# Performance work log

Hardware: AMD Instinct MI355X
Metric: run time of the kernel (lower is better)

The kernel has to match this reference:

```python
import jax, jax.numpy as jnp
import numpy as np

HIDDEN = 768
N_HEADS = 12
HEAD_DIM = HIDDEN // N_HEADS  # 64
SEQ = 2048
BATCH = 2
ROPE_BASE = 10000.0


def _rope_cos_sin(seq_len, head_dim):
    inv_freq = 1.0 / (ROPE_BASE ** (jnp.arange(0, head_dim, 2, dtype=jnp.float32) / head_dim))
    t = jnp.arange(seq_len, dtype=jnp.float32)
    freqs = jnp.einsum('s,d->sd', t, inv_freq)          # [S, D/2]
    emb = jnp.concatenate([freqs, freqs], axis=-1)      # [S, D]
    return jnp.cos(emb), jnp.sin(emb)


def _rotate_half(x):
    x1, x2 = jnp.split(x, 2, axis=-1)
    return jnp.concatenate([-x2, x1], axis=-1)


def setup_inputs() -> dict:
    key = jax.random.key(0)
    ks = jax.random.split(key, 6)
    scale = 1.0 / np.sqrt(HIDDEN)
    hidden_states = jax.random.normal(ks[0], (BATCH, SEQ, HIDDEN), dtype=jnp.float32)
    wq = jax.random.normal(ks[1], (HIDDEN, HIDDEN), dtype=jnp.float32) * scale
    wk = jax.random.normal(ks[2], (HIDDEN, HIDDEN), dtype=jnp.float32) * scale
    wv = jax.random.normal(ks[3], (HIDDEN, HIDDEN), dtype=jnp.float32) * scale
    wo = jax.random.normal(ks[4], (HIDDEN, HIDDEN), dtype=jnp.float32) * scale
    # additive causal mask: 0 on/below diagonal, large negative above
    causal = jnp.triu(jnp.full((SEQ, SEQ), -1e9, dtype=jnp.float32), k=1)
    attn_mask = causal[None, None, :, :]
    return {"hidden_states": hidden_states, "wq": wq, "wk": wk, "wv": wv,
            "wo": wo, "attn_mask": attn_mask}


def reference(hidden_states, wq, wk, wv, wo, attn_mask):
    B, S, _ = hidden_states.shape
    # projections (nn.Linear: x @ W.T)
    def proj(w):
        y = jnp.einsum('bsh,oh->bso', hidden_states, w)
        return y.reshape(B, S, N_HEADS, HEAD_DIM).transpose(0, 2, 1, 3)  # [B,H,S,D]
    q, k, v = proj(wq), proj(wk), proj(wv)
    cos, sin = _rope_cos_sin(S, HEAD_DIM)  # [S, D]
    cos = cos[None, None, :, :].astype(hidden_states.dtype)
    sin = sin[None, None, :, :].astype(hidden_states.dtype)
    q = q * cos + _rotate_half(q) * sin
    k = k * cos + _rotate_half(k) * sin
    scores = jnp.einsum('bhqd,bhkd->bhqk', q, k) / np.sqrt(HEAD_DIM)
    scores = scores + attn_mask
    probs = jax.nn.softmax(scores.astype(jnp.float32), axis=-1).astype(q.dtype)
    out = jnp.einsum('bhqk,bhkd->bhqd', probs, v)
    out = out.transpose(0, 2, 1, 3).reshape(B, S, HIDDEN)
    return jnp.einsum('bsh,oh->bso', out, wo)
```

## Files before the change

### kernel.cpp

```cpp
#include <hip/hip_runtime.h>

typedef unsigned short u16;
typedef short short8 __attribute__((ext_vector_type(8)));
typedef float f32x4 __attribute__((ext_vector_type(4)));

static_assert(sizeof(short8) == 16, "short8 must be 16B");

__device__ __forceinline__ u16 f2bf(float f) {
  unsigned u = __float_as_uint(f);
  u += 0x7FFFu + ((u >> 16) & 1u);
  return (u16)(u >> 16);
}
__device__ __forceinline__ float bf2f(u16 h) { return __uint_as_float(((unsigned)h) << 16); }

__device__ __forceinline__ f32x4 mfma_bf16(short8 a, short8 b, f32x4 c) {
  return __builtin_amdgcn_mfma_f32_16x16x32_bf16(a, b, c, 0, 0, 0);
}

__device__ __forceinline__ void gload_lds16(const void* g, void* l) {
  __builtin_amdgcn_global_load_lds((__attribute__((address_space(1))) void*)g,
                                   (__attribute__((address_space(3))) void*)l, 16, 0, 0);
}

__device__ __forceinline__ float exp2v(float x) {
  float r; asm("v_exp_f32 %0, %1" : "=v"(r) : "v"(x)); return r;
}
__device__ __forceinline__ unsigned cvtpk(float lo, float hi) {
  unsigned r; asm("v_cvt_pk_bf16_f32 %0, %1, %2" : "=v"(r) : "v"(lo), "v"(hi)); return r;
}
__device__ __forceinline__ f32x4 vmax4(f32x4 a, f32x4 b) {
  f32x4 r;
  r[0] = fmaxf(a[0], b[0]); r[1] = fmaxf(a[1], b[1]);
  r[2] = fmaxf(a[2], b[2]); r[3] = fmaxf(a[3], b[3]);
  return r;
}

__global__ __launch_bounds__(256) void cvt_kernel(
    const float* __restrict__ hs, const float* __restrict__ wq, const float* __restrict__ wk,
    const float* __restrict__ wv, const float* __restrict__ wo,
    u16* __restrict__ hbf, u16* __restrict__ wbf) {
  int i = blockIdx.x * 256 + threadIdx.x;
  const float* src; u16* dst; int idx;
  if (i < 786432) {
    src = hs; dst = hbf; idx = i;
  } else {
    int j = i - 786432;
    int seg = j / 147456;
    idx = j - seg * 147456;
    src = (seg == 0) ? wq : (seg == 1) ? wk : (seg == 2) ? wv : wo;
    dst = wbf + seg * 589824;
  }
  float4 v = ((const float4*)src)[idx];
  uint2 r;
  r.x = (unsigned)f2bf(v.x) | ((unsigned)f2bf(v.y) << 16);
  r.y = (unsigned)f2bf(v.z) | ((unsigned)f2bf(v.w) << 16);
  ((uint2*)dst)[idx] = r;
}

template <int MODE>
__global__ __launch_bounds__(256, 2) void gemm_bt(
    const u16* __restrict__ A, const u16* __restrict__ Bm,
    u16* __restrict__ qb, u16* __restrict__ kb, u16* __restrict__ vtb,
    float* __restrict__ fout) {
  __shared__ __align__(16) char sm[49152];
  const int K = 768, NK = 12;
  const int t = threadIdx.x;
  const int lane = t & 63;
  const int w = t >> 6;
  const int wr = w >> 1, wc = w & 1;
  const int lrow = lane & 15, lkg = lane >> 4;

  const int l = (MODE == 0) ? ((blockIdx.x & 7) * 144 + (blockIdx.x >> 3))
                            : ((blockIdx.x & 7) * 48 + (blockIdx.x >> 3));
  const int bx = (MODE == 0) ? (l / 18) : (l / 6);
  const int by = (MODE == 0) ? (l % 18) : (l % 6);
  const int arow0 = bx * 64, brow0 = by * 128;

  f32x4 acc[2][4];
  const f32x4 z4 = {0.f, 0.f, 0.f, 0.f};
#pragma unroll
  for (int m = 0; m < 2; ++m)
#pragma unroll
    for (int n = 0; n < 4; ++n) acc[m][n] = z4;

  const int srow = t >> 3;
  const int sslot = t & 7;

  auto STAGE = [&](int ki, int b) {
    char* sA = sm + b * 24576;
    char* sB = sA + 8192;
    const int kt = ki * 64;
#pragma unroll
    for (int it = 0; it < 2; ++it) {
      int r = it * 32 + srow;
      int ls = sslot ^ (r & 7);
      gload_lds16(A + (size_t)(arow0 + r) * K + (kt + ls * 8), sA + it * 4096 + w * 1024);
    }
#pragma unroll
    for (int it = 0; it < 4; ++it) {
      int r = it * 32 + srow;
      int ls = sslot ^ (r & 7);
      gload_lds16(Bm + (size_t)(brow0 + r) * K + (kt + ls * 8), sB + it * 4096 + w * 1024);
    }
  };

  const int g0 = lrow * 128 + ((lkg ^ (lrow & 7)) << 4);
  const int g1 = g0 ^ 64;

  STAGE(0, 0);
  __syncthreads();

  for (int ki = 0; ki < NK; ++ki) {
    const int cur = ki & 1;
    if (ki + 1 < NK) STAGE(ki + 1, cur ^ 1);
    const char* sA = sm + cur * 24576;
    const char* sB = sA + 8192;
#pragma unroll
    for (int kk = 0; kk < 2; ++kk) {
      const int go = kk ? g1 : g0;
      short8 af[2], bfr[4];
#pragma unroll
      for (int m = 0; m < 2; ++m)
        af[m] = *(const short8*)(sA + wr * 4096 + m * 2048 + go);
#pragma unroll
      for (int n = 0; n < 4; ++n)
        bfr[n] = *(const short8*)(sB + wc * 8192 + n * 2048 + go);
#pragma unroll
      for (int m = 0; m < 2; ++m)
#pragma unroll
        for (int n = 0; n < 4; ++n) acc[m][n] = mfma_bf16(af[m], bfr[n], acc[m][n]);
    }
    __syncthreads();
  }

  if (MODE == 1) {
#pragma unroll
    for (int m = 0; m < 2; ++m)
#pragma unroll
      for (int n = 0; n < 4; ++n)
#pragma unroll
        for (int i = 0; i < 4; ++i) {
          int row = arow0 + wr * 32 + m * 16 + lkg * 4 + i;
          int col = brow0 + wc * 64 + n * 16 + lrow;
          fout[(size_t)row * 768 + col] = acc[m][n][i];
        }
  } else {
    const int qsel = brow0 / 768;
    if (qsel < 2) {
      u16* dst = qsel ? kb : qb;
      const float oscale = qsel ? 1.0f : 0.1803368801111244f;
      float fr[2];
      fr[0] = __expf(-0.2878231366242557f * (float)lrow);
      fr[1] = __expf(-0.2878231366242557f * (float)(16 + lrow));
      const int hh = ((brow0 - qsel * 768) >> 6) + wc;
#pragma unroll
      for (int m = 0; m < 2; ++m)
#pragma unroll
        for (int i = 0; i < 4; ++i) {
          int row = arow0 + wr * 32 + m * 16 + lkg * 4 + i;
          int b = row >> 11, s = row & 2047;
          size_t base = ((size_t)(b * 12 + hh) * 2048 + s) * 64;
#pragma unroll
          for (int n2 = 0; n2 < 2; ++n2) {
            float x1 = acc[m][n2][i], x2 = acc[m][n2 + 2][i];
            float th = (float)s * fr[n2];
            float sn, cs;
            __sincosf(th, &sn, &cs);
            dst[base + n2 * 16 + lrow]      = f2bf((x1 * cs - x2 * sn) * oscale);
            dst[base + 32 + n2 * 16 + lrow] = f2bf((x2 * cs + x1 * sn) * oscale);
          }
        }
    } else {
#pragma unroll
      for (int m = 0; m < 2; ++m)
#pragma unroll
        for (int n = 0; n < 4; ++n)
#pragma unroll
          for (int i = 0; i < 4; ++i) {
            int row = arow0 + wr * 32 + m * 16 + lkg * 4 + i;
            int col = brow0 + wc * 64 + n * 16 + lrow;
            int b = row >> 11, s = row & 2047;
            int sc = s & 31;
            int p = ((sc & 12) << 1) | ((sc & 16) >> 2) | (sc & 3);
            int s2 = (s & ~31) | p;
            int oc = col - 1536, h = oc >> 6, d = oc & 63;
            vtb[((size_t)(b * 12 + h) * 64 + d) * 2048 + s2] = f2bf(acc[m][n][i]);
          }
    }
  }
}

__global__ __launch_bounds__(256, 2) void attn_fwd(
    const u16* __restrict__ qg, const u16* __restrict__ kg,
    const u16* __restrict__ vtg, u16* __restrict__ og) {
  __shared__ __align__(16) char sm[65536];
  const int lane = threadIdx.x & 63;
  const int w = threadIdx.x >> 6;
  const int lrow = lane & 15, lkg = lane >> 4;

  const int u = blockIdx.x;
  const int xcd = u & 7, vv = u >> 3;
  const int bh = xcd * 3 + (vv % 3);
  const int qc = 31 - (vv / 3);
  const int qw = qc * 64 + w * 16;
  const int niterS = (qc + 2) >> 1;

  const u16* Q  = qg  + (size_t)bh * (2048 * 64);
  const u16* Kp = kg  + (size_t)bh * (2048 * 64);
  const u16* VT = vtg + (size_t)bh * (64 * 2048);

  short8 qf[2];
#pragma unroll
  for (int h = 0; h < 2; ++h)
    qf[h] = *(const short8*)(Q + (size_t)(qw + lrow) * 64 + h * 32 + lkg * 8);

  const f32x4 z4 = {0.f, 0.f, 0.f, 0.f};
  f32x4 o[4] = {z4, z4, z4, z4};
  float m_ = -1e30f, l_ = 0.f;

  const int a0 = lrow * 128 + ((lkg ^ (lrow & 7)) << 4);
  const int a1 = a0 ^ 64;

  const int s_rl = lane >> 3, s_p = lane & 7;
  const int r0 = w * 16 + s_rl, r1 = r0 + 8;
  const int ls = s_p ^ (r0 & 7);
  const u16* kq0 = Kp + r0 * 64 + ls * 8;
  const u16* kq1 = Kp + r1 * 64 + ls * 8;
  const u16* vq0 = VT + (size_t)r0 * 2048 + ls * 8;
  const u16* vq1 = VT + (size_t)r1 * 2048 + ls * 8;
  const int sdst = w * 2048;

  auto STAGE = [&](int tp, int b) {
    char* sk = sm + b * 32768;
#pragma unroll
    for (int h = 0; h < 2; ++h) {
      const int kvo = tp * 128 + h * 64;
      gload_lds16(kq0 + (size_t)kvo * 64, sk + h * 8192 + sdst);
      gload_lds16(kq1 + (size_t)kvo * 64, sk + h * 8192 + sdst + 1024);
      gload_lds16(vq0 + kvo, sk + 16384 + h * 8192 + sdst);
      gload_lds16(vq1 + kvo, sk + 16384 + h * 8192 + sdst + 1024);
    }
  };

  auto ITER = [&](int t, const char* sk) {
    const char* sv = sk + 16384;
    f32x4 s[2][4];
    __builtin_amdgcn_s_setprio(1);
#pragma unroll
    for (int kb = 0; kb < 4; ++kb) {
#pragma unroll
      for (int h = 0; h < 2; ++h) {
        short8 kf0 = *(const short8*)(sk + h * 8192 + kb * 2048 + a0);
        short8 kf1 = *(const short8*)(sk + h * 8192 + kb * 2048 + a1);
        s[h][kb] = mfma_bf16(kf0, qf[0], z4);
        s[h][kb] = mfma_bf16(kf1, qf[1], s[h][kb]);
      }
    }
    __builtin_amdgcn_s_setprio(0);

    if (t == niterS - 1) {
      int qa = qw + lrow, kv0 = t << 7;
#pragma unroll
      for (int h = 0; h < 2; ++h)
#pragma unroll
        for (int kb = 0; kb < 4; ++kb)
#pragma unroll
          for (int i = 0; i < 4; ++i)
            if (kv0 + h * 64 + kb * 16 + lkg * 4 + i > qa) s[h][kb][i] = -1e30f;
    }

    f32x4 m0 = vmax4(vmax4(s[0][0], s[0][1]), vmax4(s[0][2], s[0][3]));
    f32x4 m1 = vmax4(vmax4(s[1][0], s[1][1]), vmax4(s[1][2], s[1][3]));
    f32x4 m01 = vmax4(m0, m1);
    float mt = fmaxf(fmaxf(m01[0], m01[1]), fmaxf(m01[2], m01[3]));
    mt = fmaxf(mt, __shfl_xor(mt, 16));
    mt = fmaxf(mt, __shfl_xor(mt, 32));
    if (__any(mt > m_ + 8.0f)) {
      float mn = fmaxf(m_, mt);
      float sclf = exp2v(m_ - mn);
      m_ = mn;
      l_ *= sclf;
      float sc0 = __shfl(sclf, lkg * 4 + 0);
      float sc1 = __shfl(sclf, lkg * 4 + 1);
      float sc2 = __shfl(sclf, lkg * 4 + 2);
      float sc3 = __shfl(sclf, lkg * 4 + 3);
#pragma unroll
      for (int db = 0; db < 4; ++db) {
        o[db][0] *= sc0; o[db][1] *= sc1; o[db][2] *= sc2; o[db][3] *= sc3;
      }
    }
#pragma unroll
    for (int h = 0; h < 2; ++h)
#pragma unroll
      for (int kb = 0; kb < 4; ++kb)
#pragma unroll
        for (int i = 0; i < 4; ++i) s[h][kb][i] = exp2v(s[h][kb][i] - m_);
    f32x4 st = ((s[0][0] + s[0][1]) + (s[0][2] + s[0][3])) +
               ((s[1][0] + s[1][1]) + (s[1][2] + s[1][3]));
    l_ += (st[0] + st[1]) + (st[2] + st[3]);

    short8 pa[2][2];
#pragma unroll
    for (int h = 0; h < 2; ++h) {
      uint4 p0 = { cvtpk(s[h][0][0], s[h][0][1]), cvtpk(s[h][0][2], s[h][0][3]),
                   cvtpk(s[h][1][0], s[h][1][1]), cvtpk(s[h][1][2], s[h][1][3]) };
      uint4 p1 = { cvtpk(s[h][2][0], s[h][2][1]), cvtpk(s[h][2][2], s[h][2][3]),
                   cvtpk(s[h][3][0], s[h][3][1]), cvtpk(s[h][3][2], s[h][3][3]) };
      pa[h][0] = __builtin_bit_cast(short8, p0);
      pa[h][1] = __builtin_bit_cast(short8, p1);
    }

    __builtin_amdgcn_s_setprio(1);
#pragma unroll
    for (int db = 0; db < 4; ++db) {
#pragma unroll
      for (int h = 0; h < 2; ++h) {
        short8 vf0 = *(const short8*)(sv + h * 8192 + db * 2048 + a0);
        short8 vf1 = *(const short8*)(sv + h * 8192 + db * 2048 + a1);
        o[db] = mfma_bf16(pa[h][0], vf0, o[db]);
        o[db] = mfma_bf16(pa[h][1], vf1, o[db]);
      }
    }
    __builtin_amdgcn_s_setprio(0);
  };

  STAGE(0, 0);
  __syncthreads();

  for (int t = 0; t < niterS; ++t) {
    const int cur = t & 1;
    if (t + 1 < niterS) STAGE(t + 1, cur ^ 1);
    ITER(t, sm + cur * 32768);
    __syncthreads();
  }

  l_ += __shfl_xor(l_, 16);
  l_ += __shfl_xor(l_, 32);
  int b = bh / 12, h = bh - b * 12;
  float nn[4];
  nn[0] = 1.0f / __shfl(l_, lkg * 4 + 0);
  nn[1] = 1.0f / __shfl(l_, lkg * 4 + 1);
  nn[2] = 1.0f / __shfl(l_, lkg * 4 + 2);
  nn[3] = 1.0f / __shfl(l_, lkg * 4 + 3);
#pragma unroll
  for (int i = 0; i < 4; ++i) {
    int qr = qw + lkg * 4 + i;
    u16* orow = og + ((size_t)(b * 2048 + qr)) * 768 + h * 64 + lrow;
    orow[0]  = f2bf(o[0][i] * nn[i]);
    orow[16] = f2bf(o[1][i] * nn[i]);
    orow[32] = f2bf(o[2][i] * nn[i]);
    orow[48] = f2bf(o[3][i] * nn[i]);
  }
}

extern "C" void kernel_launch(void* const* d_in, const int* in_sizes, int n_in,
                              void* d_out, int out_size, void* d_ws, size_t ws_size,
                              hipStream_t stream) {
  const float* hs = (const float*)d_in[0];
  const float* wq = (const float*)d_in[1];
  const float* wk = (const float*)d_in[2];
  const float* wv = (const float*)d_in[3];
  const float* wo = (const float*)d_in[4];
  float* out = (float*)d_out;
  char* ws = (char*)d_ws;

  u16* hbf = (u16*)(ws);
  u16* wbf = (u16*)(ws + 6291456);
  u16* qb  = (u16*)(ws + 11010048);
  u16* kb  = (u16*)(ws + 17301504);
  u16* vtb = (u16*)(ws + 23592960);
  u16* ob  = (u16*)(ws + 29884416);

  cvt_kernel<<<dim3(5376), 256, 0, stream>>>(hs, wq, wk, wv, wo, hbf, wbf);
  gemm_bt<0><<<dim3(1152), 256, 0, stream>>>(hbf, wbf, qb, kb, vtb, nullptr);
  attn_fwd<<<dim3(768), 256, 0, stream>>>(qb, kb, vtb, ob);
  gemm_bt<1><<<dim3(384), 256, 0, stream>>>(ob, wbf + 1769472, nullptr, nullptr, nullptr, out);
}
```

Measured before the change: 73.23 us.

## Fuse hidden-state bf16 conversion into QKV GEMM staging and defer max shuffles

The cvt kernel no longer converts hidden_states to bf16. The QKV GEMM now loads fp32 rows directly with register loads, converts them with v_cvt_pk_bf16_f32 and writes them to LDS in swizzled order. This removes a full write and reread of the activation buffer but drops the asynchronous global-to-LDS load for the A tile, which may expose load latency, and the GEMM re-reads fp32 data once per N-tile. Separately, attention only runs the cross-lane max shuffles when some lane's local max exceeds the running max by the threshold.

```diff
diff --git a/kernel.cpp b/kernel.cpp
--- a/kernel.cpp
+++ b/kernel.cpp
@@ -11,17 +11,13 @@
   u += 0x7FFFu + ((u >> 16) & 1u);
   return (u16)(u >> 16);
 }
-__device__ __forceinline__ float bf2f(u16 h) { return __uint_as_float(((unsigned)h) << 16); }
-
 __device__ __forceinline__ f32x4 mfma_bf16(short8 a, short8 b, f32x4 c) {
   return __builtin_amdgcn_mfma_f32_16x16x32_bf16(a, b, c, 0, 0, 0);
 }
-
 __device__ __forceinline__ void gload_lds16(const void* g, void* l) {
   __builtin_amdgcn_global_load_lds((__attribute__((address_space(1))) void*)g,
                                    (__attribute__((address_space(3))) void*)l, 16, 0, 0);
 }
-
 __device__ __forceinline__ float exp2v(float x) {
   float r; asm("v_exp_f32 %0, %1" : "=v"(r) : "v"(x)); return r;
 }
@@ -36,20 +32,14 @@
 }
 
 __global__ __launch_bounds__(256) void cvt_kernel(
-    const float* __restrict__ hs, const float* __restrict__ wq, const float* __restrict__ wk,
+    const float* __restrict__ wq, const float* __restrict__ wk,
     const float* __restrict__ wv, const float* __restrict__ wo,
-    u16* __restrict__ hbf, u16* __restrict__ wbf) {
+    u16* __restrict__ wbf) {
   int i = blockIdx.x * 256 + threadIdx.x;
-  const float* src; u16* dst; int idx;
-  if (i < 786432) {
-    src = hs; dst = hbf; idx = i;
-  } else {
-    int j = i - 786432;
-    int seg = j / 147456;
-    idx = j - seg * 147456;
-    src = (seg == 0) ? wq : (seg == 1) ? wk : (seg == 2) ? wv : wo;
-    dst = wbf + seg * 589824;
-  }
+  int seg = i / 147456;
+  int idx = i - seg * 147456;
+  const float* src = (seg == 0) ? wq : (seg == 1) ? wk : (seg == 2) ? wv : wo;
+  u16* dst = wbf + seg * 589824;
   float4 v = ((const float4*)src)[idx];
   uint2 r;
   r.x = (unsigned)f2bf(v.x) | ((unsigned)f2bf(v.y) << 16);
@@ -59,7 +49,8 @@
 
 template <int MODE>
 __global__ __launch_bounds__(256, 2) void gemm_bt(
-    const u16* __restrict__ A, const u16* __restrict__ Bm,
+    const float* __restrict__ A32, const u16* __restrict__ Abf,
+    const u16* __restrict__ Bm,
     u16* __restrict__ qb, u16* __restrict__ kb, u16* __restrict__ vtb,
     float* __restrict__ fout) {
   __shared__ __align__(16) char sm[49152];
@@ -94,7 +85,15 @@
     for (int it = 0; it < 2; ++it) {
       int r = it * 32 + srow;
       int ls = sslot ^ (r & 7);
-      gload_lds16(A + (size_t)(arow0 + r) * K + (kt + ls * 8), sA + it * 4096 + w * 1024);
+      if (MODE == 0) {
+        const float4* src = (const float4*)(A32 + (size_t)(arow0 + r) * K + (kt + ls * 8));
+        float4 x0 = src[0], x1 = src[1];
+        uint4 p = { cvtpk(x0.x, x0.y), cvtpk(x0.z, x0.w),
+                    cvtpk(x1.x, x1.y), cvtpk(x1.z, x1.w) };
+        *(uint4*)(sA + r * 128 + sslot * 16) = p;
+      } else {
+        gload_lds16(Abf + (size_t)(arow0 + r) * K + (kt + ls * 8), sA + it * 4096 + w * 1024);
+      }
     }
 #pragma unroll
     for (int it = 0; it < 4; ++it) {
@@ -272,10 +271,10 @@
     f32x4 m0 = vmax4(vmax4(s[0][0], s[0][1]), vmax4(s[0][2], s[0][3]));
     f32x4 m1 = vmax4(vmax4(s[1][0], s[1][1]), vmax4(s[1][2], s[1][3]));
     f32x4 m01 = vmax4(m0, m1);
-    float mt = fmaxf(fmaxf(m01[0], m01[1]), fmaxf(m01[2], m01[3]));
-    mt = fmaxf(mt, __shfl_xor(mt, 16));
-    mt = fmaxf(mt, __shfl_xor(mt, 32));
-    if (__any(mt > m_ + 8.0f)) {
+    float mloc = fmaxf(fmaxf(m01[0], m01[1]), fmaxf(m01[2], m01[3]));
+    if (__any(mloc > m_ + 8.0f)) {
+      float mt = fmaxf(mloc, __shfl_xor(mloc, 16));
+      mt = fmaxf(mt, __shfl_xor(mt, 32));
       float mn = fmaxf(m_, mt);
       float sclf = exp2v(m_ - mn);
       m_ = mn;
@@ -364,15 +363,14 @@
   float* out = (float*)d_out;
   char* ws = (char*)d_ws;
 
-  u16* hbf = (u16*)(ws);
   u16* wbf = (u16*)(ws + 6291456);
   u16* qb  = (u16*)(ws + 11010048);
   u16* kb  = (u16*)(ws + 17301504);
   u16* vtb = (u16*)(ws + 23592960);
   u16* ob  = (u16*)(ws + 29884416);
 
-  cvt_kernel<<<dim3(5376), 256, 0, stream>>>(hs, wq, wk, wv, wo, hbf, wbf);
-  gemm_bt<0><<<dim3(1152), 256, 0, stream>>>(hbf, wbf, qb, kb, vtb, nullptr);
+  cvt_kernel<<<dim3(2304), 256, 0, stream>>>(wq, wk, wv, wo, wbf);
+  gemm_bt<0><<<dim3(1152), 256, 0, stream>>>(hs, nullptr, wbf, qb, kb, vtb, nullptr);
   attn_fwd<<<dim3(768), 256, 0, stream>>>(qb, kb, vtb, ob);
-  gemm_bt<1><<<dim3(384), 256, 0, stream>>>(ob, wbf + 1769472, nullptr, nullptr, nullptr, out);
-}
+  gemm_bt<1><<<dim3(384), 256, 0, stream>>>(nullptr, ob, wbf + 1769472, nullptr, nullptr, nullptr, out);
+}
```

After: 75.86 us. 3.6% more time.

## Split KV range of longest causal query chunks and merge with a combine kernel

Applied to the files above, without the earlier changes.

The 12 longest query chunks per head (the deepest causal rows) are split into two blocks, each covering half the KV range. Each half writes unnormalized fp32 partial outputs plus per-row max and sum to workspace, and a new combine kernel merges them with a log-sum-exp rescale. The aim is to shorten the critical path and improve load balance across the grid, at the cost of an extra launch and fp32 partial traffic. The row-max shuffle reduction is also moved inside the rescale branch so it only runs when some lane's max actually grows.

```diff
diff --git a/kernel.cpp b/kernel.cpp
--- a/kernel.cpp
+++ b/kernel.cpp
@@ -11,17 +11,13 @@
   u += 0x7FFFu + ((u >> 16) & 1u);
   return (u16)(u >> 16);
 }
-__device__ __forceinline__ float bf2f(u16 h) { return __uint_as_float(((unsigned)h) << 16); }
-
 __device__ __forceinline__ f32x4 mfma_bf16(short8 a, short8 b, f32x4 c) {
   return __builtin_amdgcn_mfma_f32_16x16x32_bf16(a, b, c, 0, 0, 0);
 }
-
 __device__ __forceinline__ void gload_lds16(const void* g, void* l) {
   __builtin_amdgcn_global_load_lds((__attribute__((address_space(1))) void*)g,
                                    (__attribute__((address_space(3))) void*)l, 16, 0, 0);
 }
-
 __device__ __forceinline__ float exp2v(float x) {
   float r; asm("v_exp_f32 %0, %1" : "=v"(r) : "v"(x)); return r;
 }
@@ -192,18 +188,24 @@
 
 __global__ __launch_bounds__(256, 2) void attn_fwd(
     const u16* __restrict__ qg, const u16* __restrict__ kg,
-    const u16* __restrict__ vtg, u16* __restrict__ og) {
+    const u16* __restrict__ vtg, u16* __restrict__ og,
+    float* __restrict__ po, float* __restrict__ pml) {
   __shared__ __align__(16) char sm[65536];
   const int lane = threadIdx.x & 63;
   const int w = threadIdx.x >> 6;
   const int lrow = lane & 15, lkg = lane >> 4;
 
   const int u = blockIdx.x;
-  const int xcd = u & 7, vv = u >> 3;
-  const int bh = xcd * 3 + (vv % 3);
-  const int qc = 31 - (vv / 3);
+  const int xcd = u & 7, v = u >> 3;
+  const int head = v / 44, tt = v % 44;
+  const int bh = xcd * 3 + head;
+  int qc, part, isSplit;
+  if (tt < 24) { isSplit = 1; qc = 31 - (tt >> 1); part = tt & 1; }
+  else         { isSplit = 0; qc = 19 - (tt - 24); part = 0; }
+  const int nTot = (qc + 2) >> 1;
+  const int t0 = (isSplit && part) ? (nTot >> 1) : 0;
+  const int t1 = isSplit ? (part ? nTot : (nTot >> 1)) : nTot;
   const int qw = qc * 64 + w * 16;
-  const int niterS = (qc + 2) >> 1;
 
   const u16* Q  = qg  + (size_t)bh * (2048 * 64);
   const u16* Kp = kg  + (size_t)bh * (2048 * 64);
@@ -258,7 +260,7 @@
     }
     __builtin_amdgcn_s_setprio(0);
 
-    if (t == niterS - 1) {
+    if (t == nTot - 1) {
       int qa = qw + lrow, kv0 = t << 7;
 #pragma unroll
       for (int h = 0; h < 2; ++h)
@@ -272,10 +274,10 @@
     f32x4 m0 = vmax4(vmax4(s[0][0], s[0][1]), vmax4(s[0][2], s[0][3]));
     f32x4 m1 = vmax4(vmax4(s[1][0], s[1][1]), vmax4(s[1][2], s[1][3]));
     f32x4 m01 = vmax4(m0, m1);
-    float mt = fmaxf(fmaxf(m01[0], m01[1]), fmaxf(m01[2], m01[3]));
-    mt = fmaxf(mt, __shfl_xor(mt, 16));
-    mt = fmaxf(mt, __shfl_xor(mt, 32));
-    if (__any(mt > m_ + 8.0f)) {
+    float mloc = fmaxf(fmaxf(m01[0], m01[1]), fmaxf(m01[2], m01[3]));
+    if (__any(mloc > m_ + 8.0f)) {
+      float mt = fmaxf(mloc, __shfl_xor(mloc, 16));
+      mt = fmaxf(mt, __shfl_xor(mt, 32));
       float mn = fmaxf(m_, mt);
       float sclf = exp2v(m_ - mn);
       m_ = mn;
@@ -324,33 +326,79 @@
     __builtin_amdgcn_s_setprio(0);
   };
 
-  STAGE(0, 0);
+  STAGE(t0, 0);
   __syncthreads();
 
-  for (int t = 0; t < niterS; ++t) {
-    const int cur = t & 1;
-    if (t + 1 < niterS) STAGE(t + 1, cur ^ 1);
+  for (int t = t0; t < t1; ++t) {
+    const int cur = (t - t0) & 1;
+    if (t + 1 < t1) STAGE(t + 1, cur ^ 1);
     ITER(t, sm + cur * 32768);
     __syncthreads();
   }
 
   l_ += __shfl_xor(l_, 16);
   l_ += __shfl_xor(l_, 32);
+
+  if (!isSplit) {
+    int b = bh / 12, h = bh - b * 12;
+    float nn[4];
+    nn[0] = 1.0f / __shfl(l_, lkg * 4 + 0);
+    nn[1] = 1.0f / __shfl(l_, lkg * 4 + 1);
+    nn[2] = 1.0f / __shfl(l_, lkg * 4 + 2);
+    nn[3] = 1.0f / __shfl(l_, lkg * 4 + 3);
+#pragma unroll
+    for (int i = 0; i < 4; ++i) {
+      int qr = qw + lkg * 4 + i;
+      u16* orow = og + ((size_t)(b * 2048 + qr)) * 768 + h * 64 + lrow;
+      orow[0]  = f2bf(o[0][i] * nn[i]);
+      orow[16] = f2bf(o[1][i] * nn[i]);
+      orow[32] = f2bf(o[2][i] * nn[i]);
+      orow[48] = f2bf(o[3][i] * nn[i]);
+    }
+  } else {
+    const int ci = qc - 20;
+    const int bi = (bh * 12 + ci) * 2 + part;
+    float* pob = po + (size_t)bi * 4096;
+#pragma unroll
+    for (int i = 0; i < 4; ++i) {
+      int row = w * 16 + lkg * 4 + i;
+      float* prow = pob + row * 64 + lrow;
+      prow[0]  = o[0][i];
+      prow[16] = o[1][i];
+      prow[32] = o[2][i];
+      prow[48] = o[3][i];
+    }
+    if (lkg == 0) {
+      float2 v2 = {m_, l_};
+      *(float2*)(pml + (size_t)(bi * 64 + w * 16 + lrow) * 2) = v2;
+    }
+  }
+}
+
+__global__ __launch_bounds__(256) void combine_kernel(
+    const float* __restrict__ po, const float* __restrict__ pml,
+    u16* __restrict__ og) {
+  const int u = blockIdx.x;
+  const int xcd = u & 7, v = u >> 3;
+  const int head = v / 192, rem = v % 192;
+  const int ci = rem / 16, rg = rem % 16;
+  const int bh = xcd * 3 + head;
+  const int qc = ci + 20;
+  const int row = rg * 4 + (threadIdx.x >> 6);
+  const int d = threadIdx.x & 63;
+
+  const int bi0 = (bh * 12 + ci) * 2;
+  float o0 = po[((size_t)bi0 * 64 + row) * 64 + d];
+  float o1 = po[((size_t)(bi0 + 1) * 64 + row) * 64 + d];
+  float2 ml0 = *(const float2*)(pml + (size_t)(bi0 * 64 + row) * 2);
+  float2 ml1 = *(const float2*)(pml + (size_t)((bi0 + 1) * 64 + row) * 2);
+  float M = fmaxf(ml0.x, ml1.x);
+  float w0 = exp2v(ml0.x - M), w1 = exp2v(ml1.x - M);
+  float val = (o0 * w0 + o1 * w1) / (ml0.y * w0 + ml1.y * w1);
+
+  int s = qc * 64 + row;
   int b = bh / 12, h = bh - b * 12;
-  float nn[4];
-  nn[0] = 1.0f / __shfl(l_, lkg * 4 + 0);
-  nn[1] = 1.0f / __shfl(l_, lkg * 4 + 1);
-  nn[2] = 1.0f / __shfl(l_, lkg * 4 + 2);
-  nn[3] = 1.0f / __shfl(l_, lkg * 4 + 3);
-#pragma unroll
-  for (int i = 0; i < 4; ++i) {
-    int qr = qw + lkg * 4 + i;
-    u16* orow = og + ((size_t)(b * 2048 + qr)) * 768 + h * 64 + lrow;
-    orow[0]  = f2bf(o[0][i] * nn[i]);
-    orow[16] = f2bf(o[1][i] * nn[i]);
-    orow[32] = f2bf(o[2][i] * nn[i]);
-    orow[48] = f2bf(o[3][i] * nn[i]);
-  }
+  og[((size_t)(b * 2048 + s)) * 768 + h * 64 + d] = f2bf(val);
 }
 
 extern "C" void kernel_launch(void* const* d_in, const int* in_sizes, int n_in,
@@ -370,9 +418,12 @@
   u16* kb  = (u16*)(ws + 17301504);
   u16* vtb = (u16*)(ws + 23592960);
   u16* ob  = (u16*)(ws + 29884416);
+  float* po  = (float*)(ws);
+  float* pml = (float*)(ws + 9437184);
 
   cvt_kernel<<<dim3(5376), 256, 0, stream>>>(hs, wq, wk, wv, wo, hbf, wbf);
   gemm_bt<0><<<dim3(1152), 256, 0, stream>>>(hbf, wbf, qb, kb, vtb, nullptr);
-  attn_fwd<<<dim3(768), 256, 0, stream>>>(qb, kb, vtb, ob);
+  attn_fwd<<<dim3(1056), 256, 0, stream>>>(qb, kb, vtb, ob, po, pml);
+  combine_kernel<<<dim3(4608), 256, 0, stream>>>(po, pml, ob);
   gemm_bt<1><<<dim3(384), 256, 0, stream>>>(ob, wbf + 1769472, nullptr, nullptr, nullptr, out);
 }
```

Measured after the change: 81.61 us. 11.4% more time.
